# Performance work log

Measured on AMD Instinct MI355X. Metric: run time of the kernel, lower is better.

The kernel has to match this reference:

```python
import jax, jax.numpy as jnp
import numpy as np

N = 30000   # nodes
E = 600000  # edges
IN = 256    # in_channels
HID = 128   # 2*out_channels
OUT = 64    # out_channels


def setup_inputs() -> dict:
    key = jax.random.key(0)
    k = jax.random.split(key, 6)
    x = jax.random.normal(k[0], (N, IN), dtype=jnp.float32)
    edge_index = jax.random.randint(k[1], (2, E), 0, N, dtype=jnp.int64)
    W1 = jax.random.normal(k[2], (IN, HID), dtype=jnp.float32) * (1.0 / np.sqrt(IN))
    b1 = jnp.zeros((HID,), dtype=jnp.float32)
    W2 = jax.random.normal(k[3], (HID, OUT), dtype=jnp.float32) * (1.0 / np.sqrt(HID))
    b2 = jnp.zeros((OUT,), dtype=jnp.float32)
    return {"x": x, "edge_index": edge_index, "W1": W1, "b1": b1, "W2": W2, "b2": b2}


def _gcn_norm(edge_index, n_nodes):
    # PyG gcn_norm with add_self_loops=True, edge_weight=1
    loop = jnp.arange(n_nodes, dtype=edge_index.dtype)
    src = jnp.concatenate([edge_index[0], loop])
    dst = jnp.concatenate([edge_index[1], loop])
    deg = jax.ops.segment_sum(jnp.ones_like(dst, dtype=jnp.float32), dst,
                              num_segments=n_nodes)
    dinv = jnp.where(deg > 0, jax.lax.rsqrt(deg), 0.0)
    norm = dinv[src] * dinv[dst]  # [E+N]
    return src, dst, norm


def _gcn_conv(h, src, dst, norm, W, b, n_nodes):
    h = h @ W                              # [N, out] linear first (PyG order)
    msg = h[src] * norm[:, None]           # gather + per-edge scale, [E+N, out]
    out = jax.ops.segment_sum(msg, dst, num_segments=n_nodes)  # scatter-add
    return out + b


def reference(x, edge_index, W1, b1, W2, b2):
    n_nodes = x.shape[0]
    src, dst, norm = _gcn_norm(edge_index, n_nodes)
    h = _gcn_conv(x, src, dst, norm, W1, b1, n_nodes)
    h = jax.nn.relu(h)
    return _gcn_conv(h, src, dst, norm, W2, b2, n_nodes)
```

## Files before the change

kernel.cpp:

```cpp
#include <hip/hip_runtime.h>


#define GCN_IN 256
#define GCN_HID 128
#define GCN_OUT 64

#define BKT 128
#define SBE 4096
#define CAP 4096
#define SRCM 0x1FFFFFFu

typedef unsigned short ushort_t;
typedef __attribute__((ext_vector_type(8))) short short8;
typedef __attribute__((ext_vector_type(8))) unsigned short ushort8;
typedef __attribute__((ext_vector_type(4))) float f32x4;

__device__ inline float bf2f(ushort_t u) {
  union { unsigned int i; float f; } x; x.i = ((unsigned int)u) << 16; return x.f;
}
__device__ inline ushort_t f2bf(float f) {
  union { float f; unsigned int i; } u; u.f = f;
  unsigned int r = u.i + 0x7FFFu + ((u.i >> 16) & 1u);
  return (ushort_t)(r >> 16);
}

__global__ __launch_bounds__(256)
void stageX_kernel(const int* __restrict__ ei, int E,
                   const void* __restrict__ W1, const void* __restrict__ W2,
                   ushort_t* __restrict__ Wt1, ushort_t* __restrict__ Wt2,
                   int* __restrict__ flags,
                   int* __restrict__ gcur, int nbin,
                   unsigned int* __restrict__ stage) {
  __shared__ int lcnt[256];
  __shared__ int cur[256];
  __shared__ int nzc, csh;
  const int t = threadIdx.x;
  const int sb = blockIdx.x;
  lcnt[t] = 0;
  if (t == 0) { nzc = 0; csh = 0; }
  __syncthreads();
  if (t < 128) {
    if (ei[2 * t + 1] != 0) atomicAdd(&nzc, 1);
    ushort_t u = ((const ushort_t*)W1)[2 * t];
    int e = (u >> 7) & 0xFF;
    if (e >= 100 && e <= 140) atomicAdd(&csh, 1);
  }
  __syncthreads();
  const bool i64 = (nzc == 0);
  const bool f32 = (csh < 64);
  if (sb == 0 && t == 0) flags[0] = f32 ? 1 : 0;

  for (int i = sb * 256 + t; i < GCN_IN * GCN_HID + GCN_HID * GCN_OUT;
       i += gridDim.x * 256) {
    if (i < GCN_IN * GCN_HID) {
      int k = i >> 7, nn = i & 127;
      float vv = f32 ? ((const float*)W1)[i] : bf2f(((const ushort_t*)W1)[i]);
      Wt1[nn * GCN_IN + k] = f2bf(vv);
    } else {
      int j = i - GCN_IN * GCN_HID;
      int k = j >> 6, nn = j & 63;
      float vv = f32 ? ((const float*)W2)[j] : bf2f(((const ushort_t*)W2)[j]);
      Wt2[nn * GCN_HID + k] = f2bf(vv);
    }
  }

  const int base = sb * SBE;
  int end = base + SBE; if (end > E) end = E;
  unsigned int p[16];
  int bk[16];
#pragma unroll
  for (int k = 0; k < 16; ++k) {
    int i = base + t + k * 256;
    bk[k] = -1;
    if (i < end) {
      int s, d;
      if (i64) { s = ei[2 * i]; d = ei[2 * E + 2 * i]; }
      else     { s = ei[i];     d = ei[E + i]; }
      p[k] = (unsigned int)s | ((unsigned int)(d & 127) << 25);
      bk[k] = d >> 7;
      atomicAdd(&lcnt[bk[k]], 1);
    }
  }
  __syncthreads();
  for (int b = t; b < nbin; b += 256) {
    int c = lcnt[b];
    cur[b] = b * CAP + (c ? atomicAdd(&gcur[b], c) : 0);
  }
  __syncthreads();
#pragma unroll
  for (int k = 0; k < 16; ++k) {
    if (bk[k] >= 0) {
      int pos = atomicAdd(&cur[bk[k]], 1);
      if (pos < (bk[k] + 1) * CAP)
        stage[pos] = p[k];
    }
  }
}

__device__ void scatter_body(char* lds,
                             const unsigned int* __restrict__ stage,
                             const int* __restrict__ gcur, int nbin,
                             int* __restrict__ csr_src,
                             int* __restrict__ row_ptr, int* __restrict__ deg,
                             float* __restrict__ dinv, int n, int b) {
  int* lcnt  = (int*)lds;
  int* lscan = lcnt + BKT;
  int* lcur  = lcnt + 2 * BKT;
  const int t = threadIdx.x;
  const int node0 = b * BKT;
  const int nn = (n - node0 < BKT) ? (n - node0) : BKT;
  const int rb = b * CAP;
  const int re = rb + gcur[b];
  if (t < BKT) lcnt[t] = 0;
  __syncthreads();
  for (int i = rb + t; i < re; i += 256)
    atomicAdd(&lcnt[stage[i] >> 25], 1);
  __syncthreads();
  if (t < BKT) lscan[t] = lcnt[t];
  __syncthreads();
  for (int off = 1; off < BKT; off <<= 1) {
    int v = 0;
    if (t < BKT && t >= off) v = lscan[t - off];
    __syncthreads();
    if (t < BKT) lscan[t] += v;
    __syncthreads();
  }
  if (t < BKT) {
    int excl = rb + lscan[t] - lcnt[t];
    lcur[t] = excl;
    if (t < nn) {
      row_ptr[node0 + t] = excl;
      deg[node0 + t] = lcnt[t];
      dinv[node0 + t] = rsqrtf((float)(lcnt[t] + 1));
    }
  }
  __syncthreads();
  for (int i = rb + t; i < re; i += 256) {
    unsigned int p = stage[i];
    int l = p >> 25;
    int pos = atomicAdd(&lcur[l], 1);
    csr_src[pos] = (int)(p & SRCM);
  }
}

__device__ void gemm1_body(char* lds, const void* __restrict__ A,
                           const ushort_t* __restrict__ Bt,
                           ushort_t* __restrict__ C, int M,
                           const int* __restrict__ flags, int bid) {
  constexpr int K = GCN_IN, NC = GCN_HID;
  constexpr int KH = 128;
  constexpr int KPC = KH / 8;
  constexpr int NT = NC / 32;
  ushort_t* As = (ushort_t*)lds;
  ushort_t* Bs = As + 32 * KH;
  const int tid = threadIdx.x;
  const int wv = tid >> 6;
  const int lane = tid & 63;
  const int ml = lane & 15;
  const int quad = lane >> 4;
  const int row0 = bid * 32;
  const int mrow = (wv & 1) * 16 + ml;
  const int ncol0 = (wv >> 1) * (NC / 2);
  const bool aF32 = (flags[0] != 0);
  f32x4 acc[NT] = {};

  for (int ch = 0; ch < K; ch += KH) {
    if (ch) __syncthreads();
    for (int c = tid; c < 32 * KPC; c += 256) {
      int r = c / KPC, cq = c % KPC;
      ushort8 o;
      if (row0 + r < M) {
        if (aF32) {
          const float* ap = (const float*)A + (size_t)(row0 + r) * K + ch + cq * 8;
          float4 f0 = *(const float4*)ap;
          float4 f1 = *(const float4*)(ap + 4);
          o[0] = f2bf(f0.x); o[1] = f2bf(f0.y); o[2] = f2bf(f0.z); o[3] = f2bf(f0.w);
          o[4] = f2bf(f1.x); o[5] = f2bf(f1.y); o[6] = f2bf(f1.z); o[7] = f2bf(f1.w);
        } else {
          o = *(const ushort8*)((const ushort_t*)A + (size_t)(row0 + r) * K + ch + cq * 8);
        }
      } else {
        o = (ushort8)0;
      }
      int byte = (cq * 16) ^ ((r & 7) << 4);
      *(ushort8*)((char*)As + r * (KH * 2) + byte) = o;
    }
    for (int c = tid; c < NC * KPC; c += 256) {
      int nr = c / KPC, cq = c % KPC;
      ushort8 o = *(const ushort8*)(Bt + (size_t)nr * K + ch + cq * 8);
      int byte = (cq * 16) ^ ((nr & 7) << 4);
      *(ushort8*)((char*)Bs + nr * (KH * 2) + byte) = o;
    }
    __syncthreads();
#pragma unroll
    for (int kt = 0; kt < KH; kt += 32) {
      int abyte = (kt * 2 + quad * 16) ^ ((mrow & 7) << 4);
      short8 af = *(const short8*)((const char*)As + mrow * (KH * 2) + abyte);
#pragma unroll
      for (int t = 0; t < NT; ++t) {
        int nr = ncol0 + t * 16 + ml;
        int bbyte = (kt * 2 + quad * 16) ^ ((nr & 7) << 4);
        short8 bf = *(const short8*)((const char*)Bs + nr * (KH * 2) + bbyte);
        acc[t] = __builtin_amdgcn_mfma_f32_16x16x32_bf16(af, bf, acc[t], 0, 0, 0);
      }
    }
  }

  const int orow = row0 + (wv & 1) * 16 + quad * 4;
#pragma unroll
  for (int t = 0; t < NT; ++t) {
    int col = ncol0 + t * 16 + ml;
#pragma unroll
    for (int r = 0; r < 4; ++r) {
      if (orow + r < M)
        C[(size_t)(orow + r) * NC + col] = f2bf(acc[t][r]);
    }
  }
}

__global__ __launch_bounds__(256)
void scatter_gemm1_kernel(const unsigned int* __restrict__ stage,
                          const int* __restrict__ gcur, int nbin,
                          int* __restrict__ csr_src,
                          int* __restrict__ row_ptr, int* __restrict__ deg,
                          float* __restrict__ dinv, int n,
                          const void* __restrict__ x,
                          const ushort_t* __restrict__ wt1,
                          ushort_t* __restrict__ h1,
                          const int* __restrict__ flags) {
  __shared__ __align__(16) char lds[32 * 128 * 2 + 128 * 128 * 2];
  const int b = blockIdx.x;
  if (b < nbin) {
    scatter_body(lds, stage, gcur, nbin, csr_src, row_ptr, deg, dinv, n, b);
  } else {
    gemm1_body(lds, x, wt1, h1, n, flags, b - nbin);
  }
}

__global__ __launch_bounds__(256)
void agg1_gemm2_kernel(const ushort_t* __restrict__ h,
                       const int* __restrict__ row_ptr,
                       const int* __restrict__ deg,
                       const int* __restrict__ csr_src,
                       const float* __restrict__ dinv,
                       const void* __restrict__ bias,
                       const ushort_t* __restrict__ wt2,
                       ushort_t* __restrict__ h2, int n,
                       const int* __restrict__ flags) {
  __shared__ __align__(16) ushort_t hagS[16 * GCN_HID];
  __shared__ __align__(16) ushort_t w2S[GCN_OUT * GCN_HID];
  const int tid = threadIdx.x;
  const int lane = tid & 63;
  const int ni = tid >> 4;
  const int v0 = blockIdx.x * 16;
  const int v = v0 + ni;
  const int q = lane & 15;
  const int gb = lane & 48;

  for (int c = tid; c < GCN_OUT * (GCN_HID / 8); c += 256) {
    int nr = c >> 4, cq = c & 15;
    ushort8 o = *(const ushort8*)(wt2 + (size_t)nr * GCN_HID + cq * 8);
    int byte = (cq * 16) ^ ((nr & 7) << 4);
    *(ushort8*)((char*)w2S + nr * (GCN_HID * 2) + byte) = o;
  }

  if (v < n) {
    float acc[8] = {};
    const int beg = row_ptr[v];
    const int end = beg + deg[v];
    for (int base = beg; base < end; base += 16) {
      int navail = end - base; if (navail > 16) navail = 16;
      int sv = 0; float dv = 0.f;
      if (base + q < end) { sv = csr_src[base + q]; dv = dinv[sv]; }
      for (int j = 0; j < navail; j += 4) {
        int s0 = __shfl(sv, gb + j + 0), s1 = __shfl(sv, gb + j + 1);
        int s2 = __shfl(sv, gb + j + 2), s3 = __shfl(sv, gb + j + 3);
        float d0 = __shfl(dv, gb + j + 0), d1 = __shfl(dv, gb + j + 1);
        float d2 = __shfl(dv, gb + j + 2), d3 = __shfl(dv, gb + j + 3);
        ushort8 hv0 = *(const ushort8*)(h + (size_t)s0 * GCN_HID + q * 8);
        ushort8 hv1 = *(const ushort8*)(h + (size_t)s1 * GCN_HID + q * 8);
        ushort8 hv2 = *(const ushort8*)(h + (size_t)s2 * GCN_HID + q * 8);
        ushort8 hv3 = *(const ushort8*)(h + (size_t)s3 * GCN_HID + q * 8);
#pragma unroll
        for (int k = 0; k < 8; ++k) {
          acc[k] = fmaf(d0, bf2f(hv0[k]), acc[k]);
          acc[k] = fmaf(d1, bf2f(hv1[k]), acc[k]);
          acc[k] = fmaf(d2, bf2f(hv2[k]), acc[k]);
          acc[k] = fmaf(d3, bf2f(hv3[k]), acc[k]);
        }
      }
    }
    float di = dinv[v];
    float sl = di * di;
    ushort8 hv = *(const ushort8*)(h + (size_t)v * GCN_HID + q * 8);
    const bool bF32 = flags[0] != 0;
    ushort8 o;
#pragma unroll
    for (int k = 0; k < 8; ++k) {
      float bv = bF32 ? ((const float*)bias)[q * 8 + k]
                      : bf2f(((const ushort_t*)bias)[q * 8 + k]);
      o[k] = f2bf(fmaxf(di * acc[k] + sl * bf2f(hv[k]) + bv, 0.f));
    }
    int byte = (q * 16) ^ ((ni & 7) << 4);
    *(ushort8*)((char*)hagS + ni * (GCN_HID * 2) + byte) = o;
  }
  __syncthreads();

  const int wv = tid >> 6;
  const int ml = lane & 15;
  const int quad = lane >> 4;
  f32x4 acc2 = {};
#pragma unroll
  for (int kt = 0; kt < GCN_HID; kt += 32) {
    int abyte = (kt * 2 + quad * 16) ^ ((ml & 7) << 4);
    short8 af = *(const short8*)((const char*)hagS + ml * (GCN_HID * 2) + abyte);
    int nr = wv * 16 + ml;
    int bbyte = (kt * 2 + quad * 16) ^ ((nr & 7) << 4);
    short8 bf = *(const short8*)((const char*)w2S + nr * (GCN_HID * 2) + bbyte);
    acc2 = __builtin_amdgcn_mfma_f32_16x16x32_bf16(af, bf, acc2, 0, 0, 0);
  }
  const int col = wv * 16 + ml;
#pragma unroll
  for (int r = 0; r < 4; ++r) {
    int row = quad * 4 + r;
    if (v0 + row < n)
      h2[(size_t)(v0 + row) * GCN_OUT + col] = f2bf(acc2[r]);
  }
}

__global__ void aggregate_out_kernel(const ushort_t* __restrict__ h,
                                     const int* __restrict__ row_ptr,
                                     const int* __restrict__ deg,
                                     const int* __restrict__ csr_src,
                                     const float* __restrict__ dinv,
                                     const void* __restrict__ bias,
                                     void* __restrict__ outp, int n,
                                     const int* __restrict__ flags) {
  const int lane = threadIdx.x & 63;
  const int v = blockIdx.x * 32 + (threadIdx.x >> 3);
  if (v >= n) return;
  const int q = lane & 7;
  const int gb = lane & 56;
  float acc[8] = {};
  const int beg = row_ptr[v];
  const int end = beg + deg[v];
  for (int base = beg; base < end; base += 8) {
    int navail = end - base; if (navail > 8) navail = 8;
    int sv = 0; float dv = 0.f;
    if (base + q < end) { sv = csr_src[base + q]; dv = dinv[sv]; }
    for (int j = 0; j < navail; j += 4) {
      int s0 = __shfl(sv, gb + j + 0), s1 = __shfl(sv, gb + j + 1);
      int s2 = __shfl(sv, gb + j + 2), s3 = __shfl(sv, gb + j + 3);
      float d0 = __shfl(dv, gb + j + 0), d1 = __shfl(dv, gb + j + 1);
      float d2 = __shfl(dv, gb + j + 2), d3 = __shfl(dv, gb + j + 3);
      ushort8 hv0 = *(const ushort8*)(h + (size_t)s0 * GCN_OUT + q * 8);
      ushort8 hv1 = *(const ushort8*)(h + (size_t)s1 * GCN_OUT + q * 8);
      ushort8 hv2 = *(const ushort8*)(h + (size_t)s2 * GCN_OUT + q * 8);
      ushort8 hv3 = *(const ushort8*)(h + (size_t)s3 * GCN_OUT + q * 8);
#pragma unroll
      for (int k = 0; k < 8; ++k) {
        acc[k] = fmaf(d0, bf2f(hv0[k]), acc[k]);
        acc[k] = fmaf(d1, bf2f(hv1[k]), acc[k]);
        acc[k] = fmaf(d2, bf2f(hv2[k]), acc[k]);
        acc[k] = fmaf(d3, bf2f(hv3[k]), acc[k]);
      }
    }
  }
  float di = dinv[v];
  float sl = di * di;
  ushort8 hv = *(const ushort8*)(h + (size_t)v * GCN_OUT + q * 8);
  const bool oF32 = flags[0] != 0;
  float r[8];
#pragma unroll
  for (int k = 0; k < 8; ++k) {
    float bv = oF32 ? ((const float*)bias)[q * 8 + k]
                    : bf2f(((const ushort_t*)bias)[q * 8 + k]);
    r[k] = di * acc[k] + sl * bf2f(hv[k]) + bv;
  }
  if (oF32) {
    float* op = (float*)outp + (size_t)v * GCN_OUT + q * 8;
    *(float4*)op = make_float4(r[0], r[1], r[2], r[3]);
    *(float4*)(op + 4) = make_float4(r[4], r[5], r[6], r[7]);
  } else {
    ushort8 o;
#pragma unroll
    for (int k = 0; k < 8; ++k) o[k] = f2bf(r[k]);
    *(ushort8*)((ushort_t*)outp + (size_t)v * GCN_OUT + q * 8) = o;
  }
}


extern "C" void kernel_launch(void* const* d_in, const int* in_sizes, int n_in,
                              void* d_out, int out_size, void* d_ws, size_t ws_size,
                              hipStream_t stream) {
  const void* x  = d_in[0];
  const int*  ei = (const int*)d_in[1];
  const void* W1 = d_in[2];
  const void* b1 = d_in[3];
  const void* W2 = d_in[4];
  const void* b2 = d_in[5];

  const int N = in_sizes[0] / GCN_IN;
  const int E = in_sizes[1] / 2;
  const int nsb  = (E + SBE - 1) / SBE;
  const int nbin = (N + BKT - 1) / BKT;

  size_t off = 0;
  auto alloc = [&](size_t bytes) -> void* {
    void* p = (char*)d_ws + off;
    off += (bytes + 255) & ~(size_t)255;
    return p;
  };
  int*          flags   = (int*)alloc(256);
  int*          gcur    = (int*)alloc(256 * 4);
  unsigned int* stage   = (unsigned int*)alloc((size_t)nbin * CAP * 4);
  int*          csr_src = (int*)alloc((size_t)nbin * CAP * 4);
  int*          row_ptr = (int*)alloc((size_t)N * 4);
  int*          deg     = (int*)alloc((size_t)N * 4);
  float*        dinv    = (float*)alloc((size_t)N * 4);
  ushort_t*     h1      = (ushort_t*)alloc((size_t)N * GCN_HID * 2);
  ushort_t*     h2      = (ushort_t*)alloc((size_t)N * GCN_OUT * 2);
  ushort_t*     wt1     = (ushort_t*)alloc((size_t)GCN_HID * GCN_IN * 2);
  ushort_t*     wt2     = (ushort_t*)alloc((size_t)GCN_OUT * GCN_HID * 2);

  hipMemsetAsync(gcur, 0, 256 * 4, stream);

  stageX_kernel<<<nsb, 256, 0, stream>>>(ei, E, W1, W2, wt1, wt2, flags,
                                         gcur, nbin, stage);

  const int nGemm1 = (N + 31) / 32;
  scatter_gemm1_kernel<<<nbin + nGemm1, 256, 0, stream>>>(
      stage, gcur, nbin, csr_src, row_ptr, deg, dinv, N, x, wt1, h1, flags);

  agg1_gemm2_kernel<<<(N + 15) / 16, 256, 0, stream>>>(
      h1, row_ptr, deg, csr_src, dinv, b1, wt2, h2, N, flags);

  aggregate_out_kernel<<<(N + 31) / 32, 256, 0, stream>>>(
      h2, row_ptr, deg, csr_src, dinv, b2, d_out, N, flags);
}
```

Before: 149.0 us.

## Reschedule CSR build across kernels and degree-sort nodes for aggregation balance

Edge staging now runs in the same launch as the first GEMM, and the bucket scatter moves into its own kernel. A small prep kernel handles the weight transpose and clears gcur, replacing the memset. The scatter kernel also builds a per-bucket permutation that orders nodes by in-degree, and both aggregation kernels process nodes in that order so lanes grouped together get similar degrees. This is meant to cut divergence and tail imbalance in the gather loops and to overlap edge staging with GEMM1. The cost is one extra launch, an O(128^2) rank loop per bucket, and scattered output writes through the permutation.

```diff
diff --git a/kernel.cpp b/kernel.cpp
--- a/kernel.cpp
+++ b/kernel.cpp
@@ -25,45 +25,50 @@
 }
 
 __global__ __launch_bounds__(256)
-void stageX_kernel(const int* __restrict__ ei, int E,
-                   const void* __restrict__ W1, const void* __restrict__ W2,
-                   ushort_t* __restrict__ Wt1, ushort_t* __restrict__ Wt2,
-                   int* __restrict__ flags,
-                   int* __restrict__ gcur, int nbin,
-                   unsigned int* __restrict__ stage) {
-  __shared__ int lcnt[256];
-  __shared__ int cur[256];
-  __shared__ int nzc, csh;
+void prep_kernel(const void* __restrict__ W1, const void* __restrict__ W2,
+                 ushort_t* __restrict__ Wt1, ushort_t* __restrict__ Wt2,
+                 int* __restrict__ flags, int* __restrict__ gcur) {
+  __shared__ int csh;
   const int t = threadIdx.x;
-  const int sb = blockIdx.x;
-  lcnt[t] = 0;
-  if (t == 0) { nzc = 0; csh = 0; }
+  if (t == 0) csh = 0;
   __syncthreads();
   if (t < 128) {
-    if (ei[2 * t + 1] != 0) atomicAdd(&nzc, 1);
     ushort_t u = ((const ushort_t*)W1)[2 * t];
     int e = (u >> 7) & 0xFF;
     if (e >= 100 && e <= 140) atomicAdd(&csh, 1);
   }
   __syncthreads();
-  const bool i64 = (nzc == 0);
   const bool f32 = (csh < 64);
-  if (sb == 0 && t == 0) flags[0] = f32 ? 1 : 0;
-
-  for (int i = sb * 256 + t; i < GCN_IN * GCN_HID + GCN_HID * GCN_OUT;
-       i += gridDim.x * 256) {
-    if (i < GCN_IN * GCN_HID) {
-      int k = i >> 7, nn = i & 127;
-      float vv = f32 ? ((const float*)W1)[i] : bf2f(((const ushort_t*)W1)[i]);
-      Wt1[nn * GCN_IN + k] = f2bf(vv);
-    } else {
-      int j = i - GCN_IN * GCN_HID;
-      int k = j >> 6, nn = j & 63;
-      float vv = f32 ? ((const float*)W2)[j] : bf2f(((const ushort_t*)W2)[j]);
-      Wt2[nn * GCN_HID + k] = f2bf(vv);
-    }
-  }
-
+  if (blockIdx.x == 0) {
+    if (t == 0) flags[0] = f32 ? 1 : 0;
+    gcur[t] = 0;
+  }
+  int i = blockIdx.x * 256 + t;
+  if (i < GCN_IN * GCN_HID) {
+    int k = i >> 7, nn = i & 127;
+    float vv = f32 ? ((const float*)W1)[i] : bf2f(((const ushort_t*)W1)[i]);
+    Wt1[nn * GCN_IN + k] = f2bf(vv);
+  } else if (i < GCN_IN * GCN_HID + GCN_HID * GCN_OUT) {
+    int j = i - GCN_IN * GCN_HID;
+    int k = j >> 6, nn = j & 63;
+    float vv = f32 ? ((const float*)W2)[j] : bf2f(((const ushort_t*)W2)[j]);
+    Wt2[nn * GCN_HID + k] = f2bf(vv);
+  }
+}
+
+__device__ void stage_body(char* lds, const int* __restrict__ ei, int E,
+                           int* __restrict__ gcur, int nbin,
+                           unsigned int* __restrict__ stage, int sb) {
+  int* lcnt = (int*)lds;
+  int* cur  = lcnt + 256;
+  int* pnzc = cur + 256;
+  const int t = threadIdx.x;
+  lcnt[t] = 0;
+  if (t == 0) *pnzc = 0;
+  __syncthreads();
+  if (t < 128 && ei[2 * t + 1] != 0) atomicAdd(pnzc, 1);
+  __syncthreads();
+  const bool i64 = (*pnzc == 0);
   const int base = sb * SBE;
   int end = base + SBE; if (end > E) end = E;
   unsigned int p[16];
@@ -94,52 +99,6 @@
       if (pos < (bk[k] + 1) * CAP)
         stage[pos] = p[k];
     }
-  }
-}
-
-__device__ void scatter_body(char* lds,
-                             const unsigned int* __restrict__ stage,
-                             const int* __restrict__ gcur, int nbin,
-                             int* __restrict__ csr_src,
-                             int* __restrict__ row_ptr, int* __restrict__ deg,
-                             float* __restrict__ dinv, int n, int b) {
-  int* lcnt  = (int*)lds;
-  int* lscan = lcnt + BKT;
-  int* lcur  = lcnt + 2 * BKT;
-  const int t = threadIdx.x;
-  const int node0 = b * BKT;
-  const int nn = (n - node0 < BKT) ? (n - node0) : BKT;
-  const int rb = b * CAP;
-  const int re = rb + gcur[b];
-  if (t < BKT) lcnt[t] = 0;
-  __syncthreads();
-  for (int i = rb + t; i < re; i += 256)
-    atomicAdd(&lcnt[stage[i] >> 25], 1);
-  __syncthreads();
-  if (t < BKT) lscan[t] = lcnt[t];
-  __syncthreads();
-  for (int off = 1; off < BKT; off <<= 1) {
-    int v = 0;
-    if (t < BKT && t >= off) v = lscan[t - off];
-    __syncthreads();
-    if (t < BKT) lscan[t] += v;
-    __syncthreads();
-  }
-  if (t < BKT) {
-    int excl = rb + lscan[t] - lcnt[t];
-    lcur[t] = excl;
-    if (t < nn) {
-      row_ptr[node0 + t] = excl;
-      deg[node0 + t] = lcnt[t];
-      dinv[node0 + t] = rsqrtf((float)(lcnt[t] + 1));
-    }
-  }
-  __syncthreads();
-  for (int i = rb + t; i < re; i += 256) {
-    unsigned int p = stage[i];
-    int l = p >> 25;
-    int pos = atomicAdd(&lcur[l], 1);
-    csr_src[pos] = (int)(p & SRCM);
   }
 }
 
@@ -219,21 +178,75 @@
 }
 
 __global__ __launch_bounds__(256)
-void scatter_gemm1_kernel(const unsigned int* __restrict__ stage,
-                          const int* __restrict__ gcur, int nbin,
-                          int* __restrict__ csr_src,
-                          int* __restrict__ row_ptr, int* __restrict__ deg,
-                          float* __restrict__ dinv, int n,
-                          const void* __restrict__ x,
-                          const ushort_t* __restrict__ wt1,
-                          ushort_t* __restrict__ h1,
-                          const int* __restrict__ flags) {
+void stage_gemm1_kernel(const int* __restrict__ ei, int E,
+                        int* __restrict__ gcur, int nbin, int nsb,
+                        unsigned int* __restrict__ stage,
+                        const void* __restrict__ x,
+                        const ushort_t* __restrict__ wt1,
+                        ushort_t* __restrict__ h1, int n,
+                        const int* __restrict__ flags) {
   __shared__ __align__(16) char lds[32 * 128 * 2 + 128 * 128 * 2];
   const int b = blockIdx.x;
-  if (b < nbin) {
-    scatter_body(lds, stage, gcur, nbin, csr_src, row_ptr, deg, dinv, n, b);
+  if (b < nsb) {
+    stage_body(lds, ei, E, gcur, nbin, stage, b);
   } else {
-    gemm1_body(lds, x, wt1, h1, n, flags, b - nbin);
+    gemm1_body(lds, x, wt1, h1, n, flags, b - nsb);
+  }
+}
+
+__global__ __launch_bounds__(256)
+void scatter_kernel(const unsigned int* __restrict__ stage,
+                    const int* __restrict__ gcur, int nbin,
+                    int* __restrict__ csr_src,
+                    int* __restrict__ row_ptr, int* __restrict__ deg,
+                    float* __restrict__ dinv, int* __restrict__ perm, int n) {
+  __shared__ int lcnt[BKT];
+  __shared__ int lscan[BKT];
+  __shared__ int lcur[BKT];
+  const int t = threadIdx.x;
+  const int b = blockIdx.x;
+  const int node0 = b * BKT;
+  const int nn = (n - node0 < BKT) ? (n - node0) : BKT;
+  const int rb = b * CAP;
+  const int re = rb + gcur[b];
+  if (t < BKT) lcnt[t] = 0;
+  __syncthreads();
+  for (int i = rb + t; i < re; i += 256)
+    atomicAdd(&lcnt[stage[i] >> 25], 1);
+  __syncthreads();
+  if (t < BKT) lscan[t] = lcnt[t];
+  __syncthreads();
+  for (int off = 1; off < BKT; off <<= 1) {
+    int v = 0;
+    if (t < BKT && t >= off) v = lscan[t - off];
+    __syncthreads();
+    if (t < BKT) lscan[t] += v;
+    __syncthreads();
+  }
+  if (t < BKT) {
+    int excl = rb + lscan[t] - lcnt[t];
+    lcur[t] = excl;
+    if (t < nn) {
+      row_ptr[node0 + t] = excl;
+      deg[node0 + t] = lcnt[t];
+      dinv[node0 + t] = rsqrtf((float)(lcnt[t] + 1));
+    }
+  }
+  __syncthreads();
+  if (t < nn) {
+    int my = lcnt[t];
+    int rank = 0;
+    for (int u = 0; u < nn; ++u) {
+      int lu = lcnt[u];
+      rank += (lu < my || (lu == my && u < t)) ? 1 : 0;
+    }
+    perm[node0 + rank] = node0 + t;
+  }
+  for (int i = rb + t; i < re; i += 256) {
+    unsigned int p = stage[i];
+    int l = p >> 25;
+    int pos = atomicAdd(&lcur[l], 1);
+    csr_src[pos] = (int)(p & SRCM);
   }
 }
 
@@ -245,26 +258,30 @@
                        const float* __restrict__ dinv,
                        const void* __restrict__ bias,
                        const ushort_t* __restrict__ wt2,
+                       const int* __restrict__ perm,
                        ushort_t* __restrict__ h2, int n,
                        const int* __restrict__ flags) {
   __shared__ __align__(16) ushort_t hagS[16 * GCN_HID];
   __shared__ __align__(16) ushort_t w2S[GCN_OUT * GCN_HID];
+  __shared__ int pv[16];
   const int tid = threadIdx.x;
   const int lane = tid & 63;
   const int ni = tid >> 4;
   const int v0 = blockIdx.x * 16;
-  const int v = v0 + ni;
   const int q = lane & 15;
   const int gb = lane & 48;
 
+  if (tid < 16) pv[tid] = (v0 + tid < n) ? perm[v0 + tid] : -1;
   for (int c = tid; c < GCN_OUT * (GCN_HID / 8); c += 256) {
     int nr = c >> 4, cq = c & 15;
     ushort8 o = *(const ushort8*)(wt2 + (size_t)nr * GCN_HID + cq * 8);
     int byte = (cq * 16) ^ ((nr & 7) << 4);
     *(ushort8*)((char*)w2S + nr * (GCN_HID * 2) + byte) = o;
   }
-
-  if (v < n) {
+  __syncthreads();
+
+  const int v = pv[ni];
+  if (v >= 0) {
     float acc[8] = {};
     const int beg = row_ptr[v];
     const int end = beg + deg[v];
@@ -322,9 +339,9 @@
   const int col = wv * 16 + ml;
 #pragma unroll
   for (int r = 0; r < 4; ++r) {
-    int row = quad * 4 + r;
-    if (v0 + row < n)
-      h2[(size_t)(v0 + row) * GCN_OUT + col] = f2bf(acc2[r]);
+    int node = pv[quad * 4 + r];
+    if (node >= 0)
+      h2[(size_t)node * GCN_OUT + col] = f2bf(acc2[r]);
   }
 }
 
@@ -334,11 +351,13 @@
                                      const int* __restrict__ csr_src,
                                      const float* __restrict__ dinv,
                                      const void* __restrict__ bias,
+                                     const int* __restrict__ perm,
                                      void* __restrict__ outp, int n,
                                      const int* __restrict__ flags) {
   const int lane = threadIdx.x & 63;
-  const int v = blockIdx.x * 32 + (threadIdx.x >> 3);
-  if (v >= n) return;
+  const int idx = blockIdx.x * 32 + (threadIdx.x >> 3);
+  if (idx >= n) return;
+  const int v = perm[idx];
   const int q = lane & 7;
   const int gb = lane & 56;
   float acc[8] = {};
@@ -418,23 +437,25 @@
   int*          row_ptr = (int*)alloc((size_t)N * 4);
   int*          deg     = (int*)alloc((size_t)N * 4);
   float*        dinv    = (float*)alloc((size_t)N * 4);
+  int*          perm    = (int*)alloc((size_t)N * 4);
   ushort_t*     h1      = (ushort_t*)alloc((size_t)N * GCN_HID * 2);
   ushort_t*     h2      = (ushort_t*)alloc((size_t)N * GCN_OUT * 2);
   ushort_t*     wt1     = (ushort_t*)alloc((size_t)GCN_HID * GCN_IN * 2);
   ushort_t*     wt2     = (ushort_t*)alloc((size_t)GCN_OUT * GCN_HID * 2);
 
-  hipMemsetAsync(gcur, 0, 256 * 4, stream);
-
-  stageX_kernel<<<nsb, 256, 0, stream>>>(ei, E, W1, W2, wt1, wt2, flags,
-                                         gcur, nbin, stage);
+  prep_kernel<<<(GCN_IN * GCN_HID + GCN_HID * GCN_OUT + 255) / 256, 256, 0, stream>>>(
+      W1, W2, wt1, wt2, flags, gcur);
 
   const int nGemm1 = (N + 31) / 32;
-  scatter_gemm1_kernel<<<nbin + nGemm1, 256, 0, stream>>>(
-      stage, gcur, nbin, csr_src, row_ptr, deg, dinv, N, x, wt1, h1, flags);
+  stage_gemm1_kernel<<<nsb + nGemm1, 256, 0, stream>>>(
+      ei, E, gcur, nbin, nsb, stage, x, wt1, h1, N, flags);
+
+  scatter_kernel<<<nbin, 256, 0, stream>>>(stage, gcur, nbin, csr_src,
+                                           row_ptr, deg, dinv, perm, N);
 
   agg1_gemm2_kernel<<<(N + 15) / 16, 256, 0, stream>>>(
-      h1, row_ptr, deg, csr_src, dinv, b1, wt2, h2, N, flags);
+      h1, row_ptr, deg, csr_src, dinv, b1, wt2, perm, h2, N, flags);
 
   aggregate_out_kernel<<<(N + 31) / 32, 256, 0, stream>>>(
-      h2, row_ptr, deg, csr_src, dinv, b2, d_out, N, flags);
-}
+      h2, row_ptr, deg, csr_src, dinv, b2, perm, d_out, N, flags);
+}
```

Measured after the change: 157.5 us. 5.7% more time.

## Prescale h2 by dinv, pad zero row, and enlarge GEMM1 tile to 64 rows

Applied to the files above, without the earlier changes.

GEMM2's epilogue now multiplies each output row by its source node's dinv, so the final aggregation becomes a plain sum with no per-edge dinv gather or shuffle. A zero sentinel row is appended to h2 so the inner loop can run a fixed unrolled count of 8 without a tail bound, and self-loop handling is folded into di*(acc+h). GEMM1 tiles grow from 32 to 64 rows per block with each wave covering all 128 columns, which halves the block count and reuses each B tile across more rows, at the cost of more LDS and accumulator registers per block. Partial neighbor groups now issue loads to the zero row, adding some wasted memory traffic.

```diff
diff --git a/kernel.cpp b/kernel.cpp
--- a/kernel.cpp
+++ b/kernel.cpp
@@ -30,7 +30,8 @@
                    ushort_t* __restrict__ Wt1, ushort_t* __restrict__ Wt2,
                    int* __restrict__ flags,
                    int* __restrict__ gcur, int nbin,
-                   unsigned int* __restrict__ stage) {
+                   unsigned int* __restrict__ stage,
+                   ushort_t* __restrict__ h2, int N) {
   __shared__ int lcnt[256];
   __shared__ int cur[256];
   __shared__ int nzc, csh;
@@ -48,7 +49,10 @@
   __syncthreads();
   const bool i64 = (nzc == 0);
   const bool f32 = (csh < 64);
-  if (sb == 0 && t == 0) flags[0] = f32 ? 1 : 0;
+  if (sb == 0) {
+    if (t == 0) flags[0] = f32 ? 1 : 0;
+    if (t < GCN_OUT) h2[(size_t)N * GCN_OUT + t] = 0;
+  }
 
   for (int i = sb * 256 + t; i < GCN_IN * GCN_HID + GCN_HID * GCN_OUT;
        i += gridDim.x * 256) {
@@ -150,23 +154,22 @@
   constexpr int K = GCN_IN, NC = GCN_HID;
   constexpr int KH = 128;
   constexpr int KPC = KH / 8;
-  constexpr int NT = NC / 32;
+  constexpr int NT = NC / 16;
   ushort_t* As = (ushort_t*)lds;
-  ushort_t* Bs = As + 32 * KH;
+  ushort_t* Bs = As + 64 * KH;
   const int tid = threadIdx.x;
   const int wv = tid >> 6;
   const int lane = tid & 63;
   const int ml = lane & 15;
   const int quad = lane >> 4;
-  const int row0 = bid * 32;
-  const int mrow = (wv & 1) * 16 + ml;
-  const int ncol0 = (wv >> 1) * (NC / 2);
+  const int row0 = bid * 64;
+  const int mrow = wv * 16 + ml;
   const bool aF32 = (flags[0] != 0);
   f32x4 acc[NT] = {};
 
   for (int ch = 0; ch < K; ch += KH) {
     if (ch) __syncthreads();
-    for (int c = tid; c < 32 * KPC; c += 256) {
+    for (int c = tid; c < 64 * KPC; c += 256) {
       int r = c / KPC, cq = c % KPC;
       ushort8 o;
       if (row0 + r < M) {
@@ -198,7 +201,7 @@
       short8 af = *(const short8*)((const char*)As + mrow * (KH * 2) + abyte);
 #pragma unroll
       for (int t = 0; t < NT; ++t) {
-        int nr = ncol0 + t * 16 + ml;
+        int nr = t * 16 + ml;
         int bbyte = (kt * 2 + quad * 16) ^ ((nr & 7) << 4);
         short8 bf = *(const short8*)((const char*)Bs + nr * (KH * 2) + bbyte);
         acc[t] = __builtin_amdgcn_mfma_f32_16x16x32_bf16(af, bf, acc[t], 0, 0, 0);
@@ -206,10 +209,10 @@
     }
   }
 
-  const int orow = row0 + (wv & 1) * 16 + quad * 4;
+  const int orow = row0 + wv * 16 + quad * 4;
 #pragma unroll
   for (int t = 0; t < NT; ++t) {
-    int col = ncol0 + t * 16 + ml;
+    int col = t * 16 + ml;
 #pragma unroll
     for (int r = 0; r < 4; ++r) {
       if (orow + r < M)
@@ -228,7 +231,7 @@
                           const ushort_t* __restrict__ wt1,
                           ushort_t* __restrict__ h1,
                           const int* __restrict__ flags) {
-  __shared__ __align__(16) char lds[32 * 128 * 2 + 128 * 128 * 2];
+  __shared__ __align__(16) char lds[64 * 128 * 2 + 128 * 128 * 2];
   const int b = blockIdx.x;
   if (b < nbin) {
     scatter_body(lds, stage, gcur, nbin, csr_src, row_ptr, deg, dinv, n, b);
@@ -323,8 +326,10 @@
 #pragma unroll
   for (int r = 0; r < 4; ++r) {
     int row = quad * 4 + r;
-    if (v0 + row < n)
-      h2[(size_t)(v0 + row) * GCN_OUT + col] = f2bf(acc2[r]);
+    if (v0 + row < n) {
+      float dsc = dinv[v0 + row];
+      h2[(size_t)(v0 + row) * GCN_OUT + col] = f2bf(acc2[r] * dsc);
+    }
   }
 }
 
@@ -345,29 +350,26 @@
   const int beg = row_ptr[v];
   const int end = beg + deg[v];
   for (int base = beg; base < end; base += 8) {
-    int navail = end - base; if (navail > 8) navail = 8;
-    int sv = 0; float dv = 0.f;
-    if (base + q < end) { sv = csr_src[base + q]; dv = dinv[sv]; }
-    for (int j = 0; j < navail; j += 4) {
+    int sv = n;
+    if (base + q < end) sv = csr_src[base + q];
+#pragma unroll
+    for (int j = 0; j < 8; j += 4) {
       int s0 = __shfl(sv, gb + j + 0), s1 = __shfl(sv, gb + j + 1);
       int s2 = __shfl(sv, gb + j + 2), s3 = __shfl(sv, gb + j + 3);
-      float d0 = __shfl(dv, gb + j + 0), d1 = __shfl(dv, gb + j + 1);
-      float d2 = __shfl(dv, gb + j + 2), d3 = __shfl(dv, gb + j + 3);
       ushort8 hv0 = *(const ushort8*)(h + (size_t)s0 * GCN_OUT + q * 8);
       ushort8 hv1 = *(const ushort8*)(h + (size_t)s1 * GCN_OUT + q * 8);
       ushort8 hv2 = *(const ushort8*)(h + (size_t)s2 * GCN_OUT + q * 8);
       ushort8 hv3 = *(const ushort8*)(h + (size_t)s3 * GCN_OUT + q * 8);
 #pragma unroll
       for (int k = 0; k < 8; ++k) {
-        acc[k] = fmaf(d0, bf2f(hv0[k]), acc[k]);
-        acc[k] = fmaf(d1, bf2f(hv1[k]), acc[k]);
-        acc[k] = fmaf(d2, bf2f(hv2[k]), acc[k]);
-        acc[k] = fmaf(d3, bf2f(hv3[k]), acc[k]);
+        acc[k] += bf2f(hv0[k]);
+        acc[k] += bf2f(hv1[k]);
+        acc[k] += bf2f(hv2[k]);
+        acc[k] += bf2f(hv3[k]);
       }
     }
   }
   float di = dinv[v];
-  float sl = di * di;
   ushort8 hv = *(const ushort8*)(h + (size_t)v * GCN_OUT + q * 8);
   const bool oF32 = flags[0] != 0;
   float r[8];
@@ -375,7 +377,7 @@
   for (int k = 0; k < 8; ++k) {
     float bv = oF32 ? ((const float*)bias)[q * 8 + k]
                     : bf2f(((const ushort_t*)bias)[q * 8 + k]);
-    r[k] = di * acc[k] + sl * bf2f(hv[k]) + bv;
+    r[k] = di * (acc[k] + bf2f(hv[k])) + bv;
   }
   if (oF32) {
     float* op = (float*)outp + (size_t)v * GCN_OUT + q * 8;
@@ -419,16 +421,16 @@
   int*          deg     = (int*)alloc((size_t)N * 4);
   float*        dinv    = (float*)alloc((size_t)N * 4);
   ushort_t*     h1      = (ushort_t*)alloc((size_t)N * GCN_HID * 2);
-  ushort_t*     h2      = (ushort_t*)alloc((size_t)N * GCN_OUT * 2);
+  ushort_t*     h2      = (ushort_t*)alloc((size_t)(N + 1) * GCN_OUT * 2);
   ushort_t*     wt1     = (ushort_t*)alloc((size_t)GCN_HID * GCN_IN * 2);
   ushort_t*     wt2     = (ushort_t*)alloc((size_t)GCN_OUT * GCN_HID * 2);
 
   hipMemsetAsync(gcur, 0, 256 * 4, stream);
 
   stageX_kernel<<<nsb, 256, 0, stream>>>(ei, E, W1, W2, wt1, wt2, flags,
-                                         gcur, nbin, stage);
-
-  const int nGemm1 = (N + 31) / 32;
+                                         gcur, nbin, stage, h2, N);
+
+  const int nGemm1 = (N + 63) / 64;
   scatter_gemm1_kernel<<<nbin + nGemm1, 256, 0, stream>>>(
       stage, gcur, nbin, csr_src, row_ptr, deg, dinv, N, x, wt1, h1, flags);
 
```

Measured after the change: 149.7 us, median of 2. Within noise of the previous version (+0.5%).
